# Kernel tuning notes

Measured on AMD Instinct MI355X. Metric: run time of the kernel, lower is better.

## Reference

```python
import jax, jax.numpy as jnp
import numpy as np

T, B, D, H, A = 256, 512, 128, 128, 8
RUN_COUNT = 1000

def _orth(k, shape, scale):
    w = jax.random.normal(k, shape, jnp.float32)
    q, r = jnp.linalg.qr(w)
    q = q * jnp.sign(jnp.diag(r))[None, :]
    return scale * q

def setup_inputs() -> dict:
    key = jax.random.key(0)
    ks = jax.random.split(key, 12)
    return {
        'hidden': jnp.zeros((B, H), jnp.float32),
        'obs': jax.random.normal(ks[0], (T, B, D), jnp.float32),
        'dones': (jax.random.randint(ks[1], (T, B), 0, 10) == 0),
        'mean_obs': jax.random.normal(ks[2], (D,), jnp.float32) * 0.1,
        'welford_S': jax.random.uniform(ks[3], (D,), jnp.float32) * RUN_COUNT,
        'running_count': RUN_COUNT,
        'W_emb': _orth(ks[4], (D, H), float(np.sqrt(2.0))), 'b_emb': jnp.zeros((H,), jnp.float32),
        'Wi': jax.random.normal(ks[5], (H, 3 * H), jnp.float32) / np.sqrt(H),
        'Wh': jax.random.normal(ks[6], (H, 3 * H), jnp.float32) / np.sqrt(H),
        'bh': jnp.zeros((3 * H,), jnp.float32),
        'W_act': _orth(ks[7], (H, H), 2.0), 'b_act': jnp.zeros((H,), jnp.float32),
        'W_alpha': _orth(ks[8], (H, A), 0.01), 'b_alpha': jnp.zeros((A,), jnp.float32),
        'W_beta': _orth(ks[9], (H, A), 0.01), 'b_beta': jnp.zeros((A,), jnp.float32),
    }

def _welford(M0, S0, count0, xs):
    # sequential Welford update over stacked rows, as in the original lax.scan
    def step(carry, x):
        M, S, c = carry
        c = c + 1.0
        M_new = M + (x - M) / c
        S_new = S + (x - M) * (x - M_new)
        return (M_new, S_new, c), None
    (M, S, c), _ = jax.lax.scan(step, (M0, S0, jnp.asarray(count0, jnp.float32)), xs)
    return M, S, c

def reference(hidden, obs, dones, mean_obs, welford_S, running_count,
              W_emb, b_emb, Wi, Wh, bh, W_act, b_act, W_alpha, b_alpha, W_beta, b_beta):
    # --- running-stat normalization (running_count > 0 branch) ---
    stacked = obs.reshape(-1, obs.shape[-1])  # [T*B, D]
    M, S, c = _welford(mean_obs, welford_S, running_count, stacked)
    var = S / (c - 1.0)
    obs_n = (obs - M) / (jnp.sqrt(var) + 1e-8)
    # --- embedding MLP ---
    emb = jax.nn.relu(obs_n @ W_emb + b_emb)  # [T, B, H]
    # --- GRU scan over time; precompute input-side gate projections (no input bias, flax GRUCell) ---
    xg = emb @ Wi  # [T, B, 3H]
    def gru_step(h, inp):
        x3, reset = inp
        h = jnp.where(reset[:, None], 0.0, h)  # reset carry where done
        hg = h @ Wh + bh
        xr, xz, xn = jnp.split(x3, 3, axis=-1)
        hr, hz, hn = jnp.split(hg, 3, axis=-1)
        r = jax.nn.sigmoid(xr + hr)
        z = jax.nn.sigmoid(xz + hz)
        n = jnp.tanh(xn + r * hn)
        h_new = (1.0 - z) * n + z * h
        return h_new, h_new
    h_last, ys = jax.lax.scan(gru_step, hidden, (xg, dones))  # ys: [T, B, H]
    # --- policy heads ---
    act = jax.nn.relu(ys @ W_act + b_act)
    alpha = jax.nn.softplus(act @ W_alpha + b_alpha) + 1.0
    beta = jax.nn.softplus(act @ W_beta + b_beta) + 1.0
    return h_last, alpha, beta, M, S
```

## Files before the change

kernel.cpp:

```cpp
#include <hip/hip_runtime.h>

#define T_DIM 256
#define B_DIM 512
#define D_DIM 128
#define H_DIM 128
#define A_DIM 8
#define N_ROWS (T_DIM*B_DIM)
#define NT (N_ROWS/16)
#define NWIN 16
#define WLEN 16
#define LOG2E 1.4426950408889634f

typedef __attribute__((ext_vector_type(4))) float f32x4;
typedef __attribute__((ext_vector_type(8))) short bf16x8;
typedef __attribute__((ext_vector_type(4))) short bf16x4;
typedef __attribute__((ext_vector_type(8))) _Float16 f16x8;
typedef __attribute__((ext_vector_type(4))) unsigned u32x4;
typedef __attribute__((ext_vector_type(2))) unsigned u32x2;

#define OFF_PSUM   0ull
#define OFF_PSQ    1048576ull
#define OFF_STATM  2097152ull
#define OFF_STATI  2097664ull
#define OFF_WEMB   2098176ull
#define OFF_WI     2130944ull
#define OFF_WH     2229248ull
#define OFF_WACT   2425856ull
#define OFF_WHEAD  2458624ull
#define OFF_TLO    2462720ull
#define OFF_UH     2464768ull
#define OFF_XG     4194304ull
#define OFF_YS     104857600ull

#define OUT_H      0
#define OUT_ALPHA  65536
#define OUT_BETA   1114112
#define OUT_M      2162688
#define OUT_S      2162816

__device__ inline short f2bf(float x){
  union { float f; unsigned u; } v; v.f = x;
  unsigned r = v.u + 0x7FFFu + ((v.u>>16)&1u);
  return (short)(r>>16);
}
__device__ inline float bf2f(short h){
  union { unsigned u; float f; } v; v.u = ((unsigned)(unsigned short)h)<<16; return v.f;
}

__device__ inline int swz(int row, int col){ return row*136 + col; }

__device__ inline unsigned cvtpk_bf16(float lo, float hi){
  unsigned r;
  asm("v_cvt_pk_bf16_f32 %0, %1, %2" : "=v"(r) : "v"(lo), "v"(hi));
  return r;
}

__global__ __launch_bounds__(256) void k_partial(const float* __restrict__ obs,
                                                 double* __restrict__ psum,
                                                 double* __restrict__ psq){
  int tid = threadIdx.x; int col = tid & 127; int rh = tid >> 7;
  double s = 0.0, q = 0.0;
  for (int r = blockIdx.x*2 + rh; r < N_ROWS; r += 2048){
    float v = obs[(size_t)r*D_DIM + col];
    s += (double)v; q += (double)v*(double)v;
  }
  __shared__ double ls[256], lq[256];
  ls[tid]=s; lq[tid]=q; __syncthreads();
  if (rh==0){
    psum[(size_t)blockIdx.x*128 + col] = ls[tid] + ls[tid+128];
    psq [(size_t)blockIdx.x*128 + col] = lq[tid] + lq[tid+128];
  }
}

__global__ __launch_bounds__(1024) void k_stats(const double* __restrict__ psum,
                                                const double* __restrict__ psq,
                                                const float* __restrict__ mean_obs,
                                                const float* __restrict__ welfS,
                                                const int* __restrict__ runcnt,
                                                float* __restrict__ outM, float* __restrict__ outS,
                                                float* __restrict__ wsM,  float* __restrict__ wsI){
  int tid = threadIdx.x; int col = tid & 127; int seg = tid >> 7;
  double s=0.0, q=0.0;
  for (int b=seg; b<1024; b+=8){ s += psum[(size_t)b*128+col]; q += psq[(size_t)b*128+col]; }
  __shared__ double ls[1024], lq[1024];
  ls[tid]=s; lq[tid]=q; __syncthreads();
  if (seg==0){
    for (int b=1;b<8;b++){ s += ls[b*128+col]; q += lq[b*128+col]; }
    double c0 = (double)runcnt[0];
    double Nn = (double)N_ROWS;
    double n  = c0 + Nn;
    double M0 = (double)mean_obs[col], S0 = (double)welfS[col];
    double mb = s / Nn;
    double delta = mb - M0;
    double M = M0 + delta * Nn / n;
    double M2b = q - Nn*mb*mb;
    double S = S0 + M2b + delta*delta*c0*Nn/n;
    double var = S / (n - 1.0);
    float inv = (float)(1.0/(sqrt(var)+1e-8));
    outM[col] = (float)M; outS[col] = (float)S;
    wsM[col]  = (float)M; wsI[col]  = inv;
  }
}

__global__ void k_pack_all(const float* __restrict__ W_emb, const float* __restrict__ Wi,
                           const float* __restrict__ Wh,    const float* __restrict__ W_act,
                           const float* __restrict__ W_al,  const float* __restrict__ W_be,
                           short* __restrict__ Bemb, short* __restrict__ BWi,
                           short* __restrict__ BWh,  short* __restrict__ Bact,
                           short* __restrict__ Bhead){
  int gidx = blockIdx.x*256 + threadIdx.x;
  if (gidx >= 133120) return;
  if (gidx >= 131072){
    int idx = gidx - 131072;
    int j = idx & 7, lane = (idx>>3)&63, kb = (idx>>9)&3;
    int k = kb*32 + (lane>>4)*8 + j;
    int n = lane & 15;
    float wv = (n<8) ? W_al[(size_t)k*8 + n] : W_be[(size_t)k*8 + (n-8)];
    Bhead[idx] = f2bf(wv);
    return;
  }
  const float* src; short* dst; int C; int fmt; int idx;
  if (gidx < 16384)      { src=W_emb; dst=Bemb; C=128; fmt=0; idx=gidx; }
  else if (gidx < 65536) { src=Wi;    dst=BWi;  C=384; fmt=0; idx=gidx-16384; }
  else if (gidx < 114688){ src=Wh;    dst=BWh;  C=384; fmt=1; idx=gidx-65536; }
  else                   { src=W_act; dst=Bact; C=128; fmt=0; idx=gidx-114688; }
  int j = idx & 7, lane = (idx>>3)&63, kb = (idx>>9)&3, ct = idx>>11;
  int k = kb*32 + (lane>>4)*8 + j;
  int n = ct*16 + (lane&15);
  float wv = src[(size_t)k*C + n];
  short h;
  if (fmt==0) h = f2bf(wv);
  else {
    wv *= (n < 256) ? LOG2E : (2.f*LOG2E);
    union { _Float16 hf; short s; } u; u.hf = (_Float16)wv; h = u.s;
  }
  dst[idx] = h;
}

__global__ __launch_bounds__(512) void k_sched(const unsigned char* __restrict__ dones,
                                               int* __restrict__ tlo,
                                               unsigned char* __restrict__ usehid){
  int k = blockIdx.x;
  int b = threadIdx.x;
  int t0 = 0, uh = 1;
  if (k > 0){
    for (int t = WLEN*k; t >= 0; t--){
      if (dones[(size_t)t*B_DIM + b]){ t0 = t; uh = 0; break; }
    }
  }
  usehid[k*B_DIM + b] = (unsigned char)uh;
  __shared__ int red[512];
  red[b] = t0; __syncthreads();
  if (b < 32){
    int m = red[b*16];
    #pragma unroll
    for (int i=1;i<16;i++) m = min(m, red[b*16+i]);
    tlo[k*32 + b] = m;
  }
}

__global__ __launch_bounds__(512) void k_embxg(const float* __restrict__ obs,
                                               const float* __restrict__ wsM,
                                               const float* __restrict__ wsI,
                                               const short* __restrict__ Bemb,
                                               const float* __restrict__ b_emb,
                                               const short* __restrict__ BWi,
                                               const float* __restrict__ bh,
                                               short* __restrict__ xgpk){
  int tid=threadIdx.x, w=tid>>6, lane=tid&63, q=lane>>4, l=lane&15;
  int rt = blockIdx.x;
  int r0 = rt*16;
  __shared__ __align__(16) short obsL[16*136];
  __shared__ __align__(16) short embL[16*136];

  {
    int row = tid>>5, seg = tid&31;
    f32x4 o = *(const f32x4*)(obs + (size_t)(r0+row)*D_DIM + seg*4);
    f32x4 m = *(const f32x4*)(wsM + seg*4);
    f32x4 iv= *(const f32x4*)(wsI + seg*4);
    bf16x4 v;
    v[0]=f2bf((o[0]-m[0])*iv[0]); v[1]=f2bf((o[1]-m[1])*iv[1]);
    v[2]=f2bf((o[2]-m[2])*iv[2]); v[3]=f2bf((o[3]-m[3])*iv[3]);
    *(bf16x4*)&obsL[swz(row, seg*4)] = v;
  }
  __syncthreads();

  bf16x8 A[4];
  #pragma unroll
  for (int kb=0;kb<4;kb++) A[kb] = *(const bf16x8*)&obsL[swz(l, kb*32+q*8)];

  const bf16x8* BE = (const bf16x8*)Bemb;
  f32x4 accE = {0.f,0.f,0.f,0.f};
  #pragma unroll
  for (int kb=0;kb<4;kb++)
    accE = __builtin_amdgcn_mfma_f32_16x16x32_bf16(A[kb], BE[(w*4+kb)*64+lane], accE, 0,0,0);
  {
    float bb = b_emb[w*16 + l];
    #pragma unroll
    for (int r2=0;r2<4;r2++){
      float e = accE[r2] + bb; e = e>0.f ? e : 0.f;
      int b = q*4+r2;
      embL[swz(b, w*16+l)] = f2bf(e);
    }
  }
  __syncthreads();

  bf16x8 A2[4];
  #pragma unroll
  for (int kb=0;kb<4;kb++) A2[kb] = *(const bf16x8*)&embL[swz(l, kb*32+q*8)];

  const bf16x8* BW = (const bf16x8*)BWi;
  u32x2* xg8 = (u32x2*)xgpk;
  #pragma unroll
  for (int g=0; g<3; g++){
    int ct = g*8 + w;
    f32x4 acc = {0.f,0.f,0.f,0.f};
    #pragma unroll
    for (int kb=0;kb<4;kb++)
      acc = __builtin_amdgcn_mfma_f32_16x16x32_bf16(A2[kb], BW[(ct*4+kb)*64+lane], acc, 0,0,0);
    int col = ct*16 + l;
    float bb = (g<2) ? bh[col] : 0.f;
    float sc = (g<2) ? LOG2E : (2.f*LOG2E);
    u32x2 pv;
    pv[0] = cvtpk_bf16((acc[0]+bb)*sc, (acc[1]+bb)*sc);
    pv[1] = cvtpk_bf16((acc[2]+bb)*sc, (acc[3]+bb)*sc);
    xg8[((size_t)rt*24 + ct)*64 + lane] = pv;
  }
}

#define LDB(g,kb) __builtin_bit_cast(f16x8, pw4[(((g)*8+w)*4+(kb))*64+lane])
__global__
__attribute__((amdgpu_flat_work_group_size(512,512)))
__attribute__((amdgpu_waves_per_eu(4,4)))
void k_gru(const float* __restrict__ hidden,
           const unsigned char* __restrict__ dones,
           const short* __restrict__ xgpk,
           const short* __restrict__ BWh,
           const float* __restrict__ bh,
           const int* __restrict__ tlo,
           const unsigned char* __restrict__ usehid,
           short* __restrict__ yspk,
           float* __restrict__ h_last){
  int tid=threadIdx.x, w=tid>>6, lane=tid&63, q=lane>>4, l=lane&15;
  int kk = blockIdx.x >> 5, bt = blockIdx.x & 31;
  int t_out0 = kk*WLEN;
  int t_end  = t_out0 + WLEN;
  int t_start = tlo[kk*32 + bt];

  __shared__ __align__(16) _Float16 hF[2][16*136];

  const u32x4* pw4 = (const u32x4*)BWh;
  f16x8 B00 = LDB(0,0), B01 = LDB(0,1), B02 = LDB(0,2), B03 = LDB(0,3);
  f16x8 B10 = LDB(1,0), B11 = LDB(1,1), B12 = LDB(1,2), B13 = LDB(1,3);
  f16x8 B20 = LDB(2,0), B21 = LDB(2,1), B22 = LDB(2,2), B23 = LDB(2,3);

  float bh2c = bh[2*128 + w*16 + l] * (2.f*LOG2E);

  float hv[4];
  #pragma unroll
  for (int r2=0;r2<4;r2++){
    int b = bt*16 + q*4 + r2;
    hv[r2] = usehid[kk*B_DIM + b] ? hidden[(size_t)b*H_DIM + w*16 + l] : 0.f;
  }

  const bf16x4* xgt = (const bf16x4*)xgpk + (((size_t)t_start*32 + bt)*24 + w)*64 + lane;
  const unsigned char* dnp = dones + (size_t)t_start*B_DIM + bt*16 + q*4;
  bf16x4* yst = (bf16x4*)yspk + (((size_t)t_start*32 + bt)*8 + w)*64 + lane;

  bf16x4 xr_c = xgt[0], xz_c = xgt[512], xn_c = xgt[1024];
  unsigned dn_c = *(const unsigned*)dnp;
  { int a1 = (t_start+1 < t_end) ? 1 : 0; xgt += (size_t)a1*49152; dnp += a1*B_DIM; }
  bf16x4 xr_n = xgt[0], xz_n = xgt[512], xn_n = xgt[1024];
  unsigned dn_n = *(const unsigned*)dnp;

  _Float16* hA = &hF[0][0];
  _Float16* hB = &hF[1][0];
  const int wo = q*4*136 + w*16 + l;
  const int ro = l*136 + q*8;

  for (int t = t_start; t < t_end; t++){
    #pragma unroll
    for (int r2=0;r2<4;r2++){
      float hvv = ((dn_c >> (r2*8)) & 255u) ? 0.f : hv[r2];
      hv[r2] = hvv;
      hA[wo + r2*136] = (_Float16)hvv;
    }
    asm volatile("s_waitcnt lgkmcnt(0)" ::: "memory");
    __builtin_amdgcn_s_barrier();
    asm volatile("" ::: "memory");

    int a2 = (t+2 < t_end) ? 1 : 0;
    xgt += (size_t)a2 * 49152;
    dnp += a2 * B_DIM;
    bf16x4 xr_2 = xgt[0], xz_2 = xgt[512], xn_2 = xgt[1024];
    unsigned dn_2 = *(const unsigned*)dnp;

    f16x8 A0 = *(const f16x8*)(hA + ro +  0);
    f16x8 A1 = *(const f16x8*)(hA + ro + 32);
    f16x8 A2 = *(const f16x8*)(hA + ro + 64);
    f16x8 A3 = *(const f16x8*)(hA + ro + 96);

    __builtin_amdgcn_s_setprio(1);
    f32x4 acc0 = {0.f,0.f,0.f,0.f}, acc1 = {0.f,0.f,0.f,0.f}, acc2 = {0.f,0.f,0.f,0.f};
    acc0 = __builtin_amdgcn_mfma_f32_16x16x32_f16(A0, B00, acc0, 0,0,0);
    acc1 = __builtin_amdgcn_mfma_f32_16x16x32_f16(A0, B10, acc1, 0,0,0);
    acc2 = __builtin_amdgcn_mfma_f32_16x16x32_f16(A0, B20, acc2, 0,0,0);
    acc0 = __builtin_amdgcn_mfma_f32_16x16x32_f16(A1, B01, acc0, 0,0,0);
    acc1 = __builtin_amdgcn_mfma_f32_16x16x32_f16(A1, B11, acc1, 0,0,0);
    acc2 = __builtin_amdgcn_mfma_f32_16x16x32_f16(A1, B21, acc2, 0,0,0);
    acc0 = __builtin_amdgcn_mfma_f32_16x16x32_f16(A2, B02, acc0, 0,0,0);
    acc1 = __builtin_amdgcn_mfma_f32_16x16x32_f16(A2, B12, acc1, 0,0,0);
    acc2 = __builtin_amdgcn_mfma_f32_16x16x32_f16(A2, B22, acc2, 0,0,0);
    acc0 = __builtin_amdgcn_mfma_f32_16x16x32_f16(A3, B03, acc0, 0,0,0);
    acc1 = __builtin_amdgcn_mfma_f32_16x16x32_f16(A3, B13, acc1, 0,0,0);
    acc2 = __builtin_amdgcn_mfma_f32_16x16x32_f16(A3, B23, acc2, 0,0,0);
    __builtin_amdgcn_s_setprio(0);

    #pragma unroll
    for (int r2=0;r2<4;r2++){
      float xr = bf2f(xr_c[r2]), xz = bf2f(xz_c[r2]), xn = bf2f(xn_c[r2]);
      float rg = __builtin_amdgcn_rcpf(1.f + __builtin_amdgcn_exp2f(-(xr + acc0[r2])));
      float zg = __builtin_amdgcn_rcpf(1.f + __builtin_amdgcn_exp2f(-(xz + acc1[r2])));
      float e2 = __builtin_amdgcn_exp2f(xn + rg*(acc2[r2] + bh2c));
      float ng = 1.f - 2.f*__builtin_amdgcn_rcpf(e2 + 1.f);
      hv[r2] = ng + zg*(hv[r2] - ng);
    }
    if (t >= t_out0){
      u32x2 pv;
      pv[0] = cvtpk_bf16(hv[0], hv[1]);
      pv[1] = cvtpk_bf16(hv[2], hv[3]);
      *(u32x2*)yst = pv;
    }
    yst += 16384;
    xr_c = xr_n; xz_c = xz_n; xn_c = xn_n; dn_c = dn_n;
    xr_n = xr_2; xz_n = xz_2; xn_n = xn_2; dn_n = dn_2;
    _Float16* tmp = hA; hA = hB; hB = tmp;
  }

  if (kk == NWIN-1){
    #pragma unroll
    for (int r2=0;r2<4;r2++)
      h_last[(size_t)(bt*16+q*4+r2)*H_DIM + w*16 + l] = hv[r2];
  }
}

__global__ __launch_bounds__(256) void k_heads(const short* __restrict__ yspk,
                                               const short* __restrict__ Bact,
                                               const float* __restrict__ b_act,
                                               const short* __restrict__ Bhead,
                                               const float* __restrict__ b_alpha,
                                               const float* __restrict__ b_beta,
                                               float* __restrict__ alpha,
                                               float* __restrict__ beta){
  int tid=threadIdx.x, w=tid>>6, lane=tid&63, q=lane>>4, l=lane&15;
  size_t rt = (size_t)blockIdx.x*4 + w;
  __shared__ __align__(16) short tl[4][16*136];
  const bf16x4* ys4 = (const bf16x4*)yspk;
  #pragma unroll
  for (int ct=0; ct<8; ct++){
    bf16x4 v = ys4[(rt*8+ct)*64+lane];
    #pragma unroll
    for (int r2=0;r2<4;r2++){ int b=q*4+r2; tl[w][swz(b, ct*16+l)] = v[r2]; }
  }
  __syncthreads();
  bf16x8 A[4];
  #pragma unroll
  for (int kb=0;kb<4;kb++) A[kb] = *(const bf16x8*)&tl[w][swz(l, kb*32+q*8)];
  __syncthreads();
  const bf16x8* BA = (const bf16x8*)Bact;
  f32x4 accA[8];
  #pragma unroll
  for (int ct=0;ct<8;ct++){ f32x4 z = {0.f,0.f,0.f,0.f}; accA[ct]=z; }
  #pragma unroll
  for (int ct=0;ct<8;ct++)
    #pragma unroll
    for (int kb=0;kb<4;kb++)
      accA[ct] = __builtin_amdgcn_mfma_f32_16x16x32_bf16(A[kb], BA[(ct*4+kb)*64+lane], accA[ct], 0,0,0);
  #pragma unroll
  for (int ct=0;ct<8;ct++){
    int col = ct*16 + l;
    float bb = b_act[col];
    #pragma unroll
    for (int r2=0;r2<4;r2++){
      float e = accA[ct][r2] + bb; e = e>0.f ? e : 0.f;
      int b = q*4+r2;
      tl[w][swz(b, col)] = f2bf(e);
    }
  }
  __syncthreads();
  bf16x8 A2[4];
  #pragma unroll
  for (int kb=0;kb<4;kb++) A2[kb] = *(const bf16x8*)&tl[w][swz(l, kb*32+q*8)];
  const bf16x8* BHd = (const bf16x8*)Bhead;
  f32x4 acc = {0.f,0.f,0.f,0.f};
  #pragma unroll
  for (int kb=0;kb<4;kb++)
    acc = __builtin_amdgcn_mfma_f32_16x16x32_bf16(A2[kb], BHd[kb*64+lane], acc, 0,0,0);
  float bb = (l<8) ? b_alpha[l] : b_beta[l-8];
  float* dst = (l<8) ? alpha : beta;
  int cc = (l<8) ? l : l-8;
  #pragma unroll
  for (int r2=0;r2<4;r2++){
    float u = acc[r2] + bb;
    float e = __builtin_amdgcn_exp2f(-fabsf(u)*LOG2E);
    float sp = fmaxf(u,0.f) + 0.6931471805599453f*__builtin_amdgcn_logf(1.f + e);
    dst[(rt*16 + q*4 + r2)*8 + cc] = sp + 1.f;
  }
}

extern "C" void kernel_launch(void* const* d_in, const int* in_sizes, int n_in,
                              void* d_out, int out_size, void* d_ws, size_t ws_size,
                              hipStream_t stream){
  const float* hidden   = (const float*)d_in[0];
  const float* obs      = (const float*)d_in[1];
  const unsigned char* dones = (const unsigned char*)d_in[2];
  const float* mean_obs = (const float*)d_in[3];
  const float* welfS    = (const float*)d_in[4];
  const int*   runcnt   = (const int*)d_in[5];
  const float* W_emb = (const float*)d_in[6];
  const float* b_emb = (const float*)d_in[7];
  const float* Wi    = (const float*)d_in[8];
  const float* Wh    = (const float*)d_in[9];
  const float* bh    = (const float*)d_in[10];
  const float* W_act = (const float*)d_in[11];
  const float* b_act = (const float*)d_in[12];
  const float* W_al  = (const float*)d_in[13];
  const float* b_al  = (const float*)d_in[14];
  const float* W_be  = (const float*)d_in[15];
  const float* b_be  = (const float*)d_in[16];
  float* out = (float*)d_out;
  char*  ws  = (char*)d_ws;

  double* psum = (double*)(ws + OFF_PSUM);
  double* psq  = (double*)(ws + OFF_PSQ);
  float*  wsM  = (float*)(ws + OFF_STATM);
  float*  wsI  = (float*)(ws + OFF_STATI);
  short*  Bemb = (short*)(ws + OFF_WEMB);
  short*  BWi  = (short*)(ws + OFF_WI);
  short*  BWh  = (short*)(ws + OFF_WH);
  short*  Bact = (short*)(ws + OFF_WACT);
  short*  Bhead= (short*)(ws + OFF_WHEAD);
  int*    tlo  = (int*)(ws + OFF_TLO);
  unsigned char* uh = (unsigned char*)(ws + OFF_UH);
  short*  xgpk = (short*)(ws + OFF_XG);
  short*  yspk = (short*)(ws + OFF_YS);

  k_partial<<<1024,256,0,stream>>>(obs, psum, psq);
  k_stats<<<1,1024,0,stream>>>(psum, psq, mean_obs, welfS, runcnt,
                               out+OUT_M, out+OUT_S, wsM, wsI);
  k_sched<<<NWIN,512,0,stream>>>(dones, tlo, uh);
  k_pack_all<<<520,256,0,stream>>>(W_emb, Wi, Wh, W_act, W_al, W_be,
                                   Bemb, BWi, BWh, Bact, Bhead);
  k_embxg<<<8192,512,0,stream>>>(obs, wsM, wsI, Bemb, b_emb, BWi, bh, xgpk);
  k_gru<<<NWIN*32,512,0,stream>>>(hidden, dones, xgpk, BWh, bh, tlo, uh,
                                  yspk, out + OUT_H);
  k_heads<<<2048,256,0,stream>>>(yspk, Bact, b_act, Bhead, b_al, b_be,
                                 out + OUT_ALPHA, out + OUT_BETA);
}
```

Baseline: 550.6 us.

## Restructure embedding kernel per-wave, lengthen GRU windows, drop barriers and setprio

k_embxg now gives each wave its own 16-row tile in private LDS and has it compute all 8 embedding and 24 gate column tiles. This replaces the block-wide __syncthreads with per-wave lgkmcnt waits, and k_heads loses its block barriers the same way. The GRU time split goes from 16 windows of 16 steps to 8 windows of 32, with waves_per_eu lowered to 2 and the s_setprio bracketing removed. Fewer, longer windows cut the number of GRU blocks and the redundant warm-up recompute, but lengthen the serial chain each block must walk.

```diff
diff --git a/kernel.cpp b/kernel.cpp
--- a/kernel.cpp
+++ b/kernel.cpp
@@ -7,8 +7,8 @@
 #define A_DIM 8
 #define N_ROWS (T_DIM*B_DIM)
 #define NT (N_ROWS/16)
-#define NWIN 16
-#define WLEN 16
+#define NWIN 8
+#define WLEN 32
 #define LOG2E 1.4426950408889634f
 
 typedef __attribute__((ext_vector_type(4))) float f32x4;
@@ -159,7 +159,7 @@
   }
 }
 
-__global__ __launch_bounds__(512) void k_embxg(const float* __restrict__ obs,
+__global__ __launch_bounds__(256) void k_embxg(const float* __restrict__ obs,
                                                const float* __restrict__ wsM,
                                                const float* __restrict__ wsI,
                                                const short* __restrict__ Bemb,
@@ -168,70 +168,79 @@
                                                const float* __restrict__ bh,
                                                short* __restrict__ xgpk){
   int tid=threadIdx.x, w=tid>>6, lane=tid&63, q=lane>>4, l=lane&15;
-  int rt = blockIdx.x;
+  int rt = blockIdx.x*4 + w;
   int r0 = rt*16;
-  __shared__ __align__(16) short obsL[16*136];
-  __shared__ __align__(16) short embL[16*136];
+  __shared__ __align__(16) short L[4][16*136];
+  short* Lw = &L[w][0];
 
   {
-    int row = tid>>5, seg = tid&31;
-    f32x4 o = *(const f32x4*)(obs + (size_t)(r0+row)*D_DIM + seg*4);
-    f32x4 m = *(const f32x4*)(wsM + seg*4);
-    f32x4 iv= *(const f32x4*)(wsI + seg*4);
-    bf16x4 v;
-    v[0]=f2bf((o[0]-m[0])*iv[0]); v[1]=f2bf((o[1]-m[1])*iv[1]);
-    v[2]=f2bf((o[2]-m[2])*iv[2]); v[3]=f2bf((o[3]-m[3])*iv[3]);
-    *(bf16x4*)&obsL[swz(row, seg*4)] = v;
-  }
-  __syncthreads();
+    int row = lane>>2, c0 = (lane&3)*32;
+    const float* op = obs + (size_t)(r0+row)*D_DIM + c0;
+    #pragma unroll
+    for (int it=0; it<8; it++){
+      f32x4 o = *(const f32x4*)(op + it*4);
+      f32x4 m = *(const f32x4*)(wsM + c0 + it*4);
+      f32x4 iv= *(const f32x4*)(wsI + c0 + it*4);
+      bf16x4 v;
+      v[0]=f2bf((o[0]-m[0])*iv[0]); v[1]=f2bf((o[1]-m[1])*iv[1]);
+      v[2]=f2bf((o[2]-m[2])*iv[2]); v[3]=f2bf((o[3]-m[3])*iv[3]);
+      *(bf16x4*)&Lw[swz(row, c0+it*4)] = v;
+    }
+  }
+  asm volatile("s_waitcnt lgkmcnt(0)" ::: "memory");
 
   bf16x8 A[4];
   #pragma unroll
-  for (int kb=0;kb<4;kb++) A[kb] = *(const bf16x8*)&obsL[swz(l, kb*32+q*8)];
+  for (int kb=0;kb<4;kb++) A[kb] = *(const bf16x8*)&Lw[swz(l, kb*32+q*8)];
+  asm volatile("s_waitcnt lgkmcnt(0)" ::: "memory");
 
   const bf16x8* BE = (const bf16x8*)Bemb;
-  f32x4 accE = {0.f,0.f,0.f,0.f};
-  #pragma unroll
-  for (int kb=0;kb<4;kb++)
-    accE = __builtin_amdgcn_mfma_f32_16x16x32_bf16(A[kb], BE[(w*4+kb)*64+lane], accE, 0,0,0);
-  {
-    float bb = b_emb[w*16 + l];
+  #pragma unroll
+  for (int ct=0; ct<8; ct++){
+    f32x4 acc = {0.f,0.f,0.f,0.f};
+    #pragma unroll
+    for (int kb=0;kb<4;kb++)
+      acc = __builtin_amdgcn_mfma_f32_16x16x32_bf16(A[kb], BE[(ct*4+kb)*64+lane], acc, 0,0,0);
+    float bb = b_emb[ct*16 + l];
     #pragma unroll
     for (int r2=0;r2<4;r2++){
-      float e = accE[r2] + bb; e = e>0.f ? e : 0.f;
-      int b = q*4+r2;
-      embL[swz(b, w*16+l)] = f2bf(e);
-    }
-  }
-  __syncthreads();
+      float e = acc[r2] + bb; e = e>0.f ? e : 0.f;
+      Lw[swz(q*4+r2, ct*16+l)] = f2bf(e);
+    }
+  }
+  asm volatile("s_waitcnt lgkmcnt(0)" ::: "memory");
 
   bf16x8 A2[4];
   #pragma unroll
-  for (int kb=0;kb<4;kb++) A2[kb] = *(const bf16x8*)&embL[swz(l, kb*32+q*8)];
+  for (int kb=0;kb<4;kb++) A2[kb] = *(const bf16x8*)&Lw[swz(l, kb*32+q*8)];
+  asm volatile("s_waitcnt lgkmcnt(0)" ::: "memory");
 
   const bf16x8* BW = (const bf16x8*)BWi;
   u32x2* xg8 = (u32x2*)xgpk;
   #pragma unroll
   for (int g=0; g<3; g++){
-    int ct = g*8 + w;
-    f32x4 acc = {0.f,0.f,0.f,0.f};
-    #pragma unroll
-    for (int kb=0;kb<4;kb++)
-      acc = __builtin_amdgcn_mfma_f32_16x16x32_bf16(A2[kb], BW[(ct*4+kb)*64+lane], acc, 0,0,0);
-    int col = ct*16 + l;
-    float bb = (g<2) ? bh[col] : 0.f;
-    float sc = (g<2) ? LOG2E : (2.f*LOG2E);
-    u32x2 pv;
-    pv[0] = cvtpk_bf16((acc[0]+bb)*sc, (acc[1]+bb)*sc);
-    pv[1] = cvtpk_bf16((acc[2]+bb)*sc, (acc[3]+bb)*sc);
-    xg8[((size_t)rt*24 + ct)*64 + lane] = pv;
+    #pragma unroll
+    for (int c8=0; c8<8; c8++){
+      int ct = g*8 + c8;
+      f32x4 acc = {0.f,0.f,0.f,0.f};
+      #pragma unroll
+      for (int kb=0;kb<4;kb++)
+        acc = __builtin_amdgcn_mfma_f32_16x16x32_bf16(A2[kb], BW[(ct*4+kb)*64+lane], acc, 0,0,0);
+      int col = ct*16 + l;
+      float bb = (g<2) ? bh[col] : 0.f;
+      float sc = (g<2) ? LOG2E : (2.f*LOG2E);
+      u32x2 pv;
+      pv[0] = cvtpk_bf16((acc[0]+bb)*sc, (acc[1]+bb)*sc);
+      pv[1] = cvtpk_bf16((acc[2]+bb)*sc, (acc[3]+bb)*sc);
+      xg8[((size_t)rt*24 + ct)*64 + lane] = pv;
+    }
   }
 }
 
 #define LDB(g,kb) __builtin_bit_cast(f16x8, pw4[(((g)*8+w)*4+(kb))*64+lane])
 __global__
 __attribute__((amdgpu_flat_work_group_size(512,512)))
-__attribute__((amdgpu_waves_per_eu(4,4)))
+__attribute__((amdgpu_waves_per_eu(2,2)))
 void k_gru(const float* __restrict__ hidden,
            const unsigned char* __restrict__ dones,
            const short* __restrict__ xgpk,
@@ -300,7 +309,6 @@
     f16x8 A2 = *(const f16x8*)(hA + ro + 64);
     f16x8 A3 = *(const f16x8*)(hA + ro + 96);
 
-    __builtin_amdgcn_s_setprio(1);
     f32x4 acc0 = {0.f,0.f,0.f,0.f}, acc1 = {0.f,0.f,0.f,0.f}, acc2 = {0.f,0.f,0.f,0.f};
     acc0 = __builtin_amdgcn_mfma_f32_16x16x32_f16(A0, B00, acc0, 0,0,0);
     acc1 = __builtin_amdgcn_mfma_f32_16x16x32_f16(A0, B10, acc1, 0,0,0);
@@ -314,7 +322,6 @@
     acc0 = __builtin_amdgcn_mfma_f32_16x16x32_f16(A3, B03, acc0, 0,0,0);
     acc1 = __builtin_amdgcn_mfma_f32_16x16x32_f16(A3, B13, acc1, 0,0,0);
     acc2 = __builtin_amdgcn_mfma_f32_16x16x32_f16(A3, B23, acc2, 0,0,0);
-    __builtin_amdgcn_s_setprio(0);
 
     #pragma unroll
     for (int r2=0;r2<4;r2++){
@@ -355,42 +362,39 @@
   int tid=threadIdx.x, w=tid>>6, lane=tid&63, q=lane>>4, l=lane&15;
   size_t rt = (size_t)blockIdx.x*4 + w;
   __shared__ __align__(16) short tl[4][16*136];
+  short* Lw = &tl[w][0];
   const bf16x4* ys4 = (const bf16x4*)yspk;
   #pragma unroll
   for (int ct=0; ct<8; ct++){
     bf16x4 v = ys4[(rt*8+ct)*64+lane];
     #pragma unroll
-    for (int r2=0;r2<4;r2++){ int b=q*4+r2; tl[w][swz(b, ct*16+l)] = v[r2]; }
-  }
-  __syncthreads();
+    for (int r2=0;r2<4;r2++) Lw[swz(q*4+r2, ct*16+l)] = v[r2];
+  }
+  asm volatile("s_waitcnt lgkmcnt(0)" ::: "memory");
   bf16x8 A[4];
   #pragma unroll
-  for (int kb=0;kb<4;kb++) A[kb] = *(const bf16x8*)&tl[w][swz(l, kb*32+q*8)];
-  __syncthreads();
+  for (int kb=0;kb<4;kb++) A[kb] = *(const bf16x8*)&Lw[swz(l, kb*32+q*8)];
+  asm volatile("s_waitcnt lgkmcnt(0)" ::: "memory");
   const bf16x8* BA = (const bf16x8*)Bact;
-  f32x4 accA[8];
-  #pragma unroll
-  for (int ct=0;ct<8;ct++){ f32x4 z = {0.f,0.f,0.f,0.f}; accA[ct]=z; }
-  #pragma unroll
-  for (int ct=0;ct<8;ct++)
+  #pragma unroll
+  for (int ct=0;ct<8;ct++){
+    f32x4 acc = {0.f,0.f,0.f,0.f};
     #pragma unroll
     for (int kb=0;kb<4;kb++)
-      accA[ct] = __builtin_amdgcn_mfma_f32_16x16x32_bf16(A[kb], BA[(ct*4+kb)*64+lane], accA[ct], 0,0,0);
-  #pragma unroll
-  for (int ct=0;ct<8;ct++){
+      acc = __builtin_amdgcn_mfma_f32_16x16x32_bf16(A[kb], BA[(ct*4+kb)*64+lane], acc, 0,0,0);
     int col = ct*16 + l;
     float bb = b_act[col];
     #pragma unroll
     for (int r2=0;r2<4;r2++){
-      float e = accA[ct][r2] + bb; e = e>0.f ? e : 0.f;
-      int b = q*4+r2;
-      tl[w][swz(b, col)] = f2bf(e);
-    }
-  }
-  __syncthreads();
+      float e = acc[r2] + bb; e = e>0.f ? e : 0.f;
+      Lw[swz(q*4+r2, col)] = f2bf(e);
+    }
+  }
+  asm volatile("s_waitcnt lgkmcnt(0)" ::: "memory");
   bf16x8 A2[4];
   #pragma unroll
-  for (int kb=0;kb<4;kb++) A2[kb] = *(const bf16x8*)&tl[w][swz(l, kb*32+q*8)];
+  for (int kb=0;kb<4;kb++) A2[kb] = *(const bf16x8*)&Lw[swz(l, kb*32+q*8)];
+  asm volatile("s_waitcnt lgkmcnt(0)" ::: "memory");
   const bf16x8* BHd = (const bf16x8*)Bhead;
   f32x4 acc = {0.f,0.f,0.f,0.f};
   #pragma unroll
@@ -451,7 +455,7 @@
   k_sched<<<NWIN,512,0,stream>>>(dones, tlo, uh);
   k_pack_all<<<520,256,0,stream>>>(W_emb, Wi, Wh, W_act, W_al, W_be,
                                    Bemb, BWi, BWh, Bact, Bhead);
-  k_embxg<<<8192,512,0,stream>>>(obs, wsM, wsI, Bemb, b_emb, BWi, bh, xgpk);
+  k_embxg<<<2048,256,0,stream>>>(obs, wsM, wsI, Bemb, b_emb, BWi, bh, xgpk);
   k_gru<<<NWIN*32,512,0,stream>>>(hidden, dones, xgpk, BWh, bh, tlo, uh,
                                   yspk, out + OUT_H);
   k_heads<<<2048,256,0,stream>>>(yspk, Bact, b_act, Bhead, b_al, b_be,
```

New measurement: 511.3 us. -7.1%, faster.
